# Optimization experiments

Hardware: AMD Instinct MI355X
Metric: run time of the kernel (lower is better)

## Reference

```python
import jax, jax.numpy as jnp
import numpy as np

N_NODES = 100000
N_FEAT = 256
HIDDEN = 16
N_CLASSES = 16
N_EDGES = 3200000


def setup_inputs() -> dict:
    key = jax.random.key(0)
    k = jax.random.split(key, 7)
    x = jax.random.normal(k[0], (N_NODES, N_FEAT), dtype=jnp.float32)
    edge_index = jax.random.randint(k[1], (2, N_EDGES), 0, N_NODES, dtype=jnp.int32)
    # GCNConv: linear (no bias) + bias added after aggregation
    s1 = 1.0 / np.sqrt(N_FEAT)
    W1 = jax.random.uniform(k[2], (N_FEAT, HIDDEN), jnp.float32, -s1, s1)
    b1 = jnp.zeros((HIDDEN,), jnp.float32)
    # SAGEConv: lin_l (on aggregated neighbors, with bias) + lin_r (root)
    s2 = 1.0 / np.sqrt(HIDDEN)
    Wl = jax.random.uniform(k[3], (HIDDEN, N_CLASSES), jnp.float32, -s2, s2)
    Wr = jax.random.uniform(k[4], (HIDDEN, N_CLASSES), jnp.float32, -s2, s2)
    b2 = jax.random.uniform(k[5], (N_CLASSES,), jnp.float32, -s2, s2)
    return {"x": x, "edge_index": edge_index, "W1": W1, "b1": b1,
            "Wl": Wl, "Wr": Wr, "b2": b2}


def reference(x, edge_index, W1, b1, Wl, Wr, b2):
    N = x.shape[0]
    src, dst = edge_index[0], edge_index[1]

    # ---- GCNConv(num_features -> hidden): transform, add self-loops,
    # symmetric normalization, sum-aggregate, add bias ----
    h = x @ W1  # [N, H]
    loop = jnp.arange(N, dtype=src.dtype)
    src2 = jnp.concatenate([src, loop])
    dst2 = jnp.concatenate([dst, loop])
    ones = jnp.ones(src2.shape[0], dtype=h.dtype)
    deg = jax.ops.segment_sum(ones, dst2, num_segments=N)  # in-degree incl. self-loop
    dinv = jnp.where(deg > 0, jax.lax.rsqrt(deg), 0.0)
    norm = dinv[src2] * dinv[dst2]  # [E+N]
    msgs = h[src2] * norm[:, None]
    h1 = jax.ops.segment_sum(msgs, dst2, num_segments=N) + b1  # [N, H]

    # ---- SAGEConv(hidden -> num_classes, aggr='mean') ----
    cnt = jax.ops.segment_sum(jnp.ones(src.shape[0], dtype=h1.dtype), dst, num_segments=N)
    agg = jax.ops.segment_sum(h1[src], dst, num_segments=N)
    agg = agg / jnp.maximum(cnt, 1.0)[:, None]  # mean over neighbors
    out = agg @ Wl + h1 @ Wr + b2  # [N, C]

    return jax.nn.log_softmax(out, axis=1)
```

## Files before the change

### kernel.cpp

```cpp
#include <hip/hip_runtime.h>
#include <cstddef>

#define NF 256
#define NH 16
#define NC 16

#define BN    128
#define BSH   7
#define BMSK  127
#define CAP   4608
#define AVLEN 32
#define ACH   (256*AVLEN)
#define NBMAX 800

typedef __attribute__((ext_vector_type(8))) short bf16x8;
typedef __attribute__((ext_vector_type(4))) float f32x4;

__device__ inline short f2bf(float f) {
    union { float f; unsigned int u; } v; v.f = f;
    const unsigned int r = v.u + 0x7FFFu + ((v.u >> 16) & 1u);
    return (short)(r >> 16);
}

__global__ __launch_bounds__(256) void bucketA_kernel(
    const int* __restrict__ src, const int* __restrict__ dst,
    unsigned int* __restrict__ bfill, unsigned int* __restrict__ bpairs,
    int E, int NBK)
{
    __shared__ unsigned int hist[NBMAX];
    __shared__ unsigned int sbase[NBMAX];
    __shared__ unsigned int gpos[NBMAX];
    __shared__ unsigned int tmp[1024];
    __shared__ unsigned int reorder[ACH];
    __shared__ unsigned short wbid[ACH];

    const int tid = threadIdx.x;
    for (int i = tid; i < NBMAX; i += 256) hist[i] = 0u;
    __syncthreads();

    const int base = blockIdx.x * ACH;
    unsigned int pv[AVLEN];
    unsigned int ps[AVLEN];
    #pragma unroll
    for (int l = 0; l < AVLEN; ++l) {
        const int e = base + l * 256 + tid;
        if (e < E) {
            const unsigned int s = (unsigned int)src[e];
            const unsigned int d = (unsigned int)dst[e];
            const unsigned int b = d >> BSH;
            pv[l] = (s << BSH) | (d & BMSK);
            const unsigned int slot = atomicAdd(&hist[b], 1u);
            ps[l] = (slot << 10) | b;
        } else {
            ps[l] = 0xFFFFFFFFu;
        }
    }
    __syncthreads();

    for (int i = tid; i < 1024; i += 256) tmp[i] = (i < NBK) ? hist[i] : 0u;
    __syncthreads();
    for (int off = 1; off < 1024; off <<= 1) {
        unsigned int v0 = 0, v1 = 0, v2 = 0, v3 = 0;
        const int i0 = tid, i1 = tid + 256, i2 = tid + 512, i3 = tid + 768;
        if (i0 >= off) v0 = tmp[i0 - off];
        if (i1 >= off) v1 = tmp[i1 - off];
        if (i2 >= off) v2 = tmp[i2 - off];
        if (i3 >= off) v3 = tmp[i3 - off];
        __syncthreads();
        tmp[i0] += v0; tmp[i1] += v1; tmp[i2] += v2; tmp[i3] += v3;
        __syncthreads();
    }
    for (int i = tid; i < NBK; i += 256) {
        const unsigned int h = hist[i];
        sbase[i] = tmp[i] - h;
        if (h) gpos[i] = atomicAdd(&bfill[i], h);
    }
    const int cc = (base + ACH <= E) ? ACH : (E - base);
    __syncthreads();

    #pragma unroll
    for (int l = 0; l < AVLEN; ++l) {
        if (ps[l] != 0xFFFFFFFFu) {
            const unsigned int b = ps[l] & 1023u;
            const unsigned int i = sbase[b] + (ps[l] >> 10);
            reorder[i] = pv[l];
            wbid[i] = (unsigned short)b;
        }
    }
    __syncthreads();

    for (int i = tid; i < cc; i += 256) {
        const unsigned int b = wbid[i];
        const unsigned int g = gpos[b] + ((unsigned int)i - sbase[b]);
        if (g < CAP) bpairs[(size_t)b * CAP + g] = reorder[i];
    }
}

__global__ __launch_bounds__(256) void bucketB_kernel(
    const unsigned int* __restrict__ bfill, unsigned int* __restrict__ bpairs,
    int* __restrict__ rowptr, int* __restrict__ cnt, float* __restrict__ dinv,
    int N)
{
    __shared__ unsigned int pairs[CAP];
    __shared__ unsigned int ssorted[CAP];
    __shared__ unsigned int hist[BN];
    __shared__ unsigned int scan[BN];
    __shared__ unsigned int cursor[BN];

    const int tid = threadIdx.x;
    const int b = blockIdx.x;
    const size_t bbase = (size_t)b * CAP;
    unsigned int m = bfill[b]; if (m > CAP) m = CAP;

    if (tid < BN) hist[tid] = 0u;
    __syncthreads();

    for (unsigned int i = tid; i < m; i += 256) {
        const unsigned int p = bpairs[bbase + i];
        pairs[i] = p;
        atomicAdd(&hist[p & BMSK], 1u);
    }
    __syncthreads();

    if (tid < BN) scan[tid] = hist[tid];
    __syncthreads();
    for (int off = 1; off < BN; off <<= 1) {
        unsigned int v = 0;
        if (tid < BN && tid >= off) v = scan[tid - off];
        __syncthreads();
        if (tid < BN) scan[tid] += v;
        __syncthreads();
    }
    if (tid < BN) cursor[tid] = scan[tid] - hist[tid];
    __syncthreads();

    for (unsigned int i = tid; i < m; i += 256) {
        const unsigned int p = pairs[i];
        const unsigned int pos = atomicAdd(&cursor[p & BMSK], 1u);
        ssorted[pos] = p >> BSH;
    }
    __syncthreads();

    for (unsigned int i = tid; i < m; i += 256)
        bpairs[bbase + i] = ssorted[i];

    if (tid < BN) {
        const int n = b * BN + tid;
        if (n < N) {
            const unsigned int h = hist[tid];
            cnt[n] = (int)h;
            dinv[n] = rsqrtf((float)h + 1.0f);
            rowptr[n] = (int)(b * CAP + (scan[tid] - h));
        }
    }
}

__global__ __launch_bounds__(256) void gemm1_mfma_kernel(
    const float* __restrict__ x, const float* __restrict__ W1,
    const float* __restrict__ dinv, float* __restrict__ hs, int N)
{
    const int lane = threadIdx.x & 63;
    const int wave = threadIdx.x >> 6;
    const int quad = lane >> 4;
    const int mn   = lane & 15;

    bf16x8 bfrag[8];
    #pragma unroll
    for (int kc = 0; kc < 8; ++kc) {
        #pragma unroll
        for (int j = 0; j < 8; ++j) {
            const int k = kc * 32 + quad * 8 + j;
            bfrag[kc][j] = f2bf(W1[k * NH + mn]);
        }
    }

    const int tile = blockIdx.x * 4 + wave;
    if (tile * 16 >= N) return;
    const int n0 = tile * 16;

    f32x4 acc = {0.f, 0.f, 0.f, 0.f};
    const float* xrow = x + (size_t)(n0 + mn) * NF + quad * 8;
    #pragma unroll
    for (int kc = 0; kc < 8; ++kc) {
        const float4 lo = *(const float4*)(xrow + kc * 32);
        const float4 hi = *(const float4*)(xrow + kc * 32 + 4);
        bf16x8 af;
        af[0] = f2bf(lo.x); af[1] = f2bf(lo.y); af[2] = f2bf(lo.z); af[3] = f2bf(lo.w);
        af[4] = f2bf(hi.x); af[5] = f2bf(hi.y); af[6] = f2bf(hi.z); af[7] = f2bf(hi.w);
        acc = __builtin_amdgcn_mfma_f32_16x16x32_bf16(af, bfrag[kc], acc, 0, 0, 0);
    }

    const float4 dv = *(const float4*)(dinv + n0 + quad * 4);
    const float d[4] = {dv.x, dv.y, dv.z, dv.w};
    #pragma unroll
    for (int r = 0; r < 4; ++r) {
        const int row = quad * 4 + r;
        hs[(size_t)(n0 + row) * NH + mn] = acc[r] * d[r];
    }
}

__global__ __launch_bounds__(256) void gcn_gather_kernel(
    const float* __restrict__ hs, const unsigned int* __restrict__ csrc,
    const int* __restrict__ rowptr, const int* __restrict__ cnt,
    const float* __restrict__ dinv, const float* __restrict__ b1,
    float* __restrict__ h1, int N)
{
    const int tid = threadIdx.x;
    const int n = blockIdx.x * 16 + (tid >> 4);
    if (n >= N) return;
    const int j = tid & 15;
    const int start = rowptr[n];
    const int end = start + cnt[n];
    float acc = hs[(size_t)n * NH + j];
    int k = start;
    for (; k + 8 <= end; k += 8) {
        const int s0 = csrc[k],   s1 = csrc[k+1], s2 = csrc[k+2], s3 = csrc[k+3];
        const int s4 = csrc[k+4], s5 = csrc[k+5], s6 = csrc[k+6], s7 = csrc[k+7];
        const float a0 = hs[(size_t)s0 * NH + j];
        const float a1 = hs[(size_t)s1 * NH + j];
        const float a2 = hs[(size_t)s2 * NH + j];
        const float a3 = hs[(size_t)s3 * NH + j];
        const float a4 = hs[(size_t)s4 * NH + j];
        const float a5 = hs[(size_t)s5 * NH + j];
        const float a6 = hs[(size_t)s6 * NH + j];
        const float a7 = hs[(size_t)s7 * NH + j];
        acc += ((a0 + a1) + (a2 + a3)) + ((a4 + a5) + (a6 + a7));
    }
    for (; k < end; ++k) acc += hs[(size_t)csrc[k] * NH + j];
    h1[(size_t)n * NH + j] = b1[j] + dinv[n] * acc;
}

__global__ __launch_bounds__(256) void sage_out_kernel(
    const float* __restrict__ h1, const unsigned int* __restrict__ csrc,
    const int* __restrict__ rowptr, const int* __restrict__ cnt,
    const float* __restrict__ Wl, const float* __restrict__ Wr,
    const float* __restrict__ b2, float* __restrict__ out, int N)
{
    __shared__ float wls[NH * NC];
    __shared__ float wrs[NH * NC];
    __shared__ float b2s[NC];
    const int tid = threadIdx.x;
    if (tid < NH * NC) { wls[tid] = Wl[tid]; wrs[tid] = Wr[tid]; }
    if (tid < NC) b2s[tid] = b2[tid];
    __syncthreads();

    const int n = blockIdx.x * 16 + (tid >> 4);
    if (n >= N) return;
    const int j = tid & 15;
    const int start = rowptr[n];
    const int deg = cnt[n];
    const int end = start + deg;

    float acc = 0.f;
    int k = start;
    for (; k + 8 <= end; k += 8) {
        const int s0 = csrc[k],   s1 = csrc[k+1], s2 = csrc[k+2], s3 = csrc[k+3];
        const int s4 = csrc[k+4], s5 = csrc[k+5], s6 = csrc[k+6], s7 = csrc[k+7];
        acc += ((h1[(size_t)s0 * NH + j] + h1[(size_t)s1 * NH + j])
              + (h1[(size_t)s2 * NH + j] + h1[(size_t)s3 * NH + j]))
             + ((h1[(size_t)s4 * NH + j] + h1[(size_t)s5 * NH + j])
              + (h1[(size_t)s6 * NH + j] + h1[(size_t)s7 * NH + j]));
    }
    for (; k < end; ++k) acc += h1[(size_t)csrc[k] * NH + j];

    const float aggj = acc / fmaxf((float)deg, 1.0f);
    const float h1j  = h1[(size_t)n * NH + j];

    float o = b2s[j];
    #pragma unroll
    for (int kk = 0; kk < NH; ++kk) {
        const float a  = __shfl(aggj, kk, 16);
        const float hh = __shfl(h1j,  kk, 16);
        o += a * wls[kk * NC + j] + hh * wrs[kk * NC + j];
    }

    float m = o;
    #pragma unroll
    for (int off = 1; off < 16; off <<= 1) m = fmaxf(m, __shfl_xor(m, off, 16));
    const float ex = expf(o - m);
    float ssum = ex;
    #pragma unroll
    for (int off = 1; off < 16; off <<= 1) ssum += __shfl_xor(ssum, off, 16);

    out[(size_t)n * NC + j] = (o - m) - logf(ssum);
}

extern "C" void kernel_launch(void* const* d_in, const int* in_sizes, int n_in,
                              void* d_out, int out_size, void* d_ws, size_t ws_size,
                              hipStream_t stream)
{
    const float* x  = (const float*)d_in[0];
    const int*   ei = (const int*)d_in[1];
    const float* W1 = (const float*)d_in[2];
    const float* b1 = (const float*)d_in[3];
    const float* Wl = (const float*)d_in[4];
    const float* Wr = (const float*)d_in[5];
    const float* b2 = (const float*)d_in[6];
    float* out = (float*)d_out;

    const int N = in_sizes[0] / NF;
    const int E = in_sizes[1] / 2;
    const int* src = ei;
    const int* dst = ei + E;

    const int NBK = (N + BN - 1) / BN;

    float* hs     = (float*)d_ws;
    float* h1     = hs + (size_t)N * NH;
    float* dinv   = h1 + (size_t)N * NH;
    int*   cnt    = (int*)(dinv + N);
    int*   rowptr = cnt + N;
    unsigned int* bfill  = (unsigned int*)(rowptr + N);
    unsigned int* bpairs = bfill + 1024;

    hipMemsetAsync(bfill, 0, (size_t)NBK * sizeof(unsigned int), stream);

    bucketA_kernel<<<(E + ACH - 1) / ACH, 256, 0, stream>>>(src, dst, bfill, bpairs, E, NBK);
    bucketB_kernel<<<NBK, 256, 0, stream>>>(bfill, bpairs, rowptr, cnt, dinv, N);

    const int tiles = (N + 15) / 16;
    gemm1_mfma_kernel<<<(tiles + 3) / 4, 256, 0, stream>>>(x, W1, dinv, hs, N);

    const int nodeBlk = (N + 15) / 16;
    gcn_gather_kernel<<<nodeBlk, 256, 0, stream>>>(hs, bpairs, rowptr, cnt, dinv, b1, h1, N);
    sage_out_kernel<<<nodeBlk, 256, 0, stream>>>(h1, bpairs, rowptr, cnt, Wl, Wr, b2, out, N);
}
```

Measured before the change: 321.7 us.

## Store intermediate node features in bf16 and shuffle-broadcast edge indices in gathers

The hidden features hs and h1 are now stored as bf16 instead of fp32, which halves the bytes touched by each random gather row in both aggregation kernels. The gather loops also change: each of the 16 lanes loads one edge index and the indices are broadcast with shuffles, replacing eight redundant per-lane index loads per step. This trades accuracy, since the intermediates are rounded to bf16 and accumulation errors may grow, for lower memory traffic and fewer index loads.

```diff
diff --git a/kernel.cpp b/kernel.cpp
--- a/kernel.cpp
+++ b/kernel.cpp
@@ -20,6 +20,10 @@
     union { float f; unsigned int u; } v; v.f = f;
     const unsigned int r = v.u + 0x7FFFu + ((v.u >> 16) & 1u);
     return (short)(r >> 16);
+}
+__device__ inline float bf2f(unsigned short u) {
+    union { unsigned int i; float f; } v; v.i = ((unsigned int)u) << 16;
+    return v.f;
 }
 
 __global__ __launch_bounds__(256) void bucketA_kernel(
@@ -157,7 +161,7 @@
 
 __global__ __launch_bounds__(256) void gemm1_mfma_kernel(
     const float* __restrict__ x, const float* __restrict__ W1,
-    const float* __restrict__ dinv, float* __restrict__ hs, int N)
+    const float* __restrict__ dinv, unsigned short* __restrict__ hs_bf, int N)
 {
     const int lane = threadIdx.x & 63;
     const int wave = threadIdx.x >> 6;
@@ -195,15 +199,15 @@
     #pragma unroll
     for (int r = 0; r < 4; ++r) {
         const int row = quad * 4 + r;
-        hs[(size_t)(n0 + row) * NH + mn] = acc[r] * d[r];
+        hs_bf[(size_t)(n0 + row) * NH + mn] = (unsigned short)f2bf(acc[r] * d[r]);
     }
 }
 
 __global__ __launch_bounds__(256) void gcn_gather_kernel(
-    const float* __restrict__ hs, const unsigned int* __restrict__ csrc,
+    const unsigned short* __restrict__ hs_bf, const unsigned int* __restrict__ csrc,
     const int* __restrict__ rowptr, const int* __restrict__ cnt,
     const float* __restrict__ dinv, const float* __restrict__ b1,
-    float* __restrict__ h1, int N)
+    unsigned short* __restrict__ h1_bf, int N)
 {
     const int tid = threadIdx.x;
     const int n = blockIdx.x * 16 + (tid >> 4);
@@ -211,27 +215,27 @@
     const int j = tid & 15;
     const int start = rowptr[n];
     const int end = start + cnt[n];
-    float acc = hs[(size_t)n * NH + j];
+
+    float acc = bf2f(hs_bf[(size_t)n * NH + j]);
     int k = start;
-    for (; k + 8 <= end; k += 8) {
-        const int s0 = csrc[k],   s1 = csrc[k+1], s2 = csrc[k+2], s3 = csrc[k+3];
-        const int s4 = csrc[k+4], s5 = csrc[k+5], s6 = csrc[k+6], s7 = csrc[k+7];
-        const float a0 = hs[(size_t)s0 * NH + j];
-        const float a1 = hs[(size_t)s1 * NH + j];
-        const float a2 = hs[(size_t)s2 * NH + j];
-        const float a3 = hs[(size_t)s3 * NH + j];
-        const float a4 = hs[(size_t)s4 * NH + j];
-        const float a5 = hs[(size_t)s5 * NH + j];
-        const float a6 = hs[(size_t)s6 * NH + j];
-        const float a7 = hs[(size_t)s7 * NH + j];
-        acc += ((a0 + a1) + (a2 + a3)) + ((a4 + a5) + (a6 + a7));
-    }
-    for (; k < end; ++k) acc += hs[(size_t)csrc[k] * NH + j];
-    h1[(size_t)n * NH + j] = b1[j] + dinv[n] * acc;
+    for (; k + 16 <= end; k += 16) {
+        const int myi = (int)csrc[k + j];
+        float s = 0.f;
+        #pragma unroll
+        for (int u = 0; u < 16; ++u) {
+            const int sidx = __shfl(myi, u, 16);
+            s += bf2f(hs_bf[(size_t)sidx * NH + j]);
+        }
+        acc += s;
+    }
+    for (; k < end; ++k)
+        acc += bf2f(hs_bf[(size_t)csrc[k] * NH + j]);
+
+    h1_bf[(size_t)n * NH + j] = (unsigned short)f2bf(b1[j] + dinv[n] * acc);
 }
 
 __global__ __launch_bounds__(256) void sage_out_kernel(
-    const float* __restrict__ h1, const unsigned int* __restrict__ csrc,
+    const unsigned short* __restrict__ h1_bf, const unsigned int* __restrict__ csrc,
     const int* __restrict__ rowptr, const int* __restrict__ cnt,
     const float* __restrict__ Wl, const float* __restrict__ Wr,
     const float* __restrict__ b2, float* __restrict__ out, int N)
@@ -253,18 +257,21 @@
 
     float acc = 0.f;
     int k = start;
-    for (; k + 8 <= end; k += 8) {
-        const int s0 = csrc[k],   s1 = csrc[k+1], s2 = csrc[k+2], s3 = csrc[k+3];
-        const int s4 = csrc[k+4], s5 = csrc[k+5], s6 = csrc[k+6], s7 = csrc[k+7];
-        acc += ((h1[(size_t)s0 * NH + j] + h1[(size_t)s1 * NH + j])
-              + (h1[(size_t)s2 * NH + j] + h1[(size_t)s3 * NH + j]))
-             + ((h1[(size_t)s4 * NH + j] + h1[(size_t)s5 * NH + j])
-              + (h1[(size_t)s6 * NH + j] + h1[(size_t)s7 * NH + j]));
-    }
-    for (; k < end; ++k) acc += h1[(size_t)csrc[k] * NH + j];
+    for (; k + 16 <= end; k += 16) {
+        const int myi = (int)csrc[k + j];
+        float s = 0.f;
+        #pragma unroll
+        for (int u = 0; u < 16; ++u) {
+            const int sidx = __shfl(myi, u, 16);
+            s += bf2f(h1_bf[(size_t)sidx * NH + j]);
+        }
+        acc += s;
+    }
+    for (; k < end; ++k)
+        acc += bf2f(h1_bf[(size_t)csrc[k] * NH + j]);
 
     const float aggj = acc / fmaxf((float)deg, 1.0f);
-    const float h1j  = h1[(size_t)n * NH + j];
+    const float h1j  = bf2f(h1_bf[(size_t)n * NH + j]);
 
     float o = b2s[j];
     #pragma unroll
@@ -305,9 +312,9 @@
 
     const int NBK = (N + BN - 1) / BN;
 
-    float* hs     = (float*)d_ws;
-    float* h1     = hs + (size_t)N * NH;
-    float* dinv   = h1 + (size_t)N * NH;
+    unsigned short* hs_bf = (unsigned short*)d_ws;
+    unsigned short* h1_bf = hs_bf + (size_t)N * NH;
+    float* dinv   = (float*)(h1_bf + (size_t)N * NH);
     int*   cnt    = (int*)(dinv + N);
     int*   rowptr = cnt + N;
     unsigned int* bfill  = (unsigned int*)(rowptr + N);
@@ -319,9 +326,9 @@
     bucketB_kernel<<<NBK, 256, 0, stream>>>(bfill, bpairs, rowptr, cnt, dinv, N);
 
     const int tiles = (N + 15) / 16;
-    gemm1_mfma_kernel<<<(tiles + 3) / 4, 256, 0, stream>>>(x, W1, dinv, hs, N);
+    gemm1_mfma_kernel<<<(tiles + 3) / 4, 256, 0, stream>>>(x, W1, dinv, hs_bf, N);
 
     const int nodeBlk = (N + 15) / 16;
-    gcn_gather_kernel<<<nodeBlk, 256, 0, stream>>>(hs, bpairs, rowptr, cnt, dinv, b1, h1, N);
-    sage_out_kernel<<<nodeBlk, 256, 0, stream>>>(h1, bpairs, rowptr, cnt, Wl, Wr, b2, out, N);
-}
+    gcn_gather_kernel<<<nodeBlk, 256, 0, stream>>>(hs_bf, bpairs, rowptr, cnt, dinv, b1, h1_bf, N);
+    sage_out_kernel<<<nodeBlk, 256, 0, stream>>>(h1_bf, bpairs, rowptr, cnt, Wl, Wr, b2, out, N);
+}
```

Result: no change. 319.2 us (-0.8%).
